# Optimization experiments

Measured on AMD Instinct MI355X. Metric: run time of the kernel, lower is better.

## Reference

```python
import jax, jax.numpy as jnp
import numpy as np
import math

TAU = 1.0  # init kwarg tau


def setup_inputs() -> dict:
    key = jax.random.key(0)
    n, m = 1024, 8192
    V = jax.random.normal(key, (n, m), dtype=jnp.float32)
    return {"V": V}


def reference(V) -> jnp.ndarray:
    n, m = V.shape
    num_rounds = math.ceil(m / n)
    # Repeat V row-blocks num_rounds times: M has shape [num_rounds*n, m]
    M = jnp.tile(V, (num_rounds, 1))

    def step(c, row):
        # Soft round-robin pick (training branch of SoftRR.__one_round)
        y = jax.nn.softmax((row - jnp.min(row) + 1.0) * c / TAU)
        c = (1.0 - y) * c
        return c, y

    c0 = jnp.ones((m,), dtype=V.dtype)
    _, R = jax.lax.scan(step, c0, M)  # R: [num_rounds*n, m]
    pi = R.reshape(num_rounds, n, m).sum(axis=0)  # [n, m]
    return pi
```

## Files before the change

kernel.cpp:

```cpp
#include <hip/hip_runtime.h>
#include <hip/hip_fp16.h>


#define N_ROWS 1024
#define M_COLS 8192
#define STEPS  8192
#define LOG2E  1.4426950408889634f

using half8  = __attribute__((ext_vector_type(8))) _Float16;
using half2v = __attribute__((ext_vector_type(2))) _Float16;
using float8 = __attribute__((ext_vector_type(8))) float;

__device__ __forceinline__ float fast_exp2(float x) {
#if __has_builtin(__builtin_amdgcn_exp2f)
  return __builtin_amdgcn_exp2f(x);
#else
  return exp2f(x);
#endif
}
__device__ __forceinline__ float fast_rcp(float x) {
#if __has_builtin(__builtin_amdgcn_rcpf)
  return __builtin_amdgcn_rcpf(x);
#else
  return 1.0f / x;
#endif
}
__device__ __forceinline__ half2v pack_f16(float y0, float y1) {
  return __builtin_bit_cast(half2v, __builtin_amdgcn_cvt_pkrtz(y0, y1));
}

template <int CTRL>
__device__ __forceinline__ float dpp_add(float x) {
  int yi = __builtin_amdgcn_update_dpp(0, __builtin_bit_cast(int, x),
                                       CTRL, 0xf, 0xf, true);
  return x + __builtin_bit_cast(float, yi);
}

__device__ __forceinline__ float wave_sum_to_lane63(float x) {
  x = dpp_add<0x111>(x);
  x = dpp_add<0x112>(x);
  x = dpp_add<0x114>(x);
  x = dpp_add<0x118>(x);
  x = dpp_add<0x142>(x);
  x = dpp_add<0x143>(x);
  return x;
}

#define BAR_LDS_ONLY() asm volatile("s_waitcnt lgkmcnt(0)\n\ts_barrier" ::: "memory")

__global__ void softrr_rowmin(const float* __restrict__ V, float* __restrict__ rmin) {
  const int row = blockIdx.x;
  const float* p = V + (size_t)row * M_COLS;
  float m = 1e30f;
  for (int j = threadIdx.x; j < M_COLS; j += 256) m = fminf(m, p[j]);
#pragma unroll
  for (int off = 32; off; off >>= 1) m = fminf(m, __shfl_xor(m, off, 64));
  __shared__ float sm[4];
  if ((threadIdx.x & 63) == 0) sm[threadIdx.x >> 6] = m;
  __syncthreads();
  if (threadIdx.x == 0) {
    rmin[row] = fminf(fminf(sm[0], sm[1]), fminf(sm[2], sm[3]));
  }
}

__global__ void softrr_prep_f32(const float* __restrict__ V, const float* __restrict__ rmin,
                                float* __restrict__ A) {
  const int idx8 = blockIdx.x * 256 + threadIdx.x;
  const int row = idx8 >> 10;
  const float mn = rmin[row];
  const float4* v4 = (const float4*)V;
  float4 va = v4[2 * idx8];
  float4 vb = v4[2 * idx8 + 1];
  float8 o;
  o[0] = (va.x - mn + 1.0f) * LOG2E;
  o[1] = (va.y - mn + 1.0f) * LOG2E;
  o[2] = (va.z - mn + 1.0f) * LOG2E;
  o[3] = (va.w - mn + 1.0f) * LOG2E;
  o[4] = (vb.x - mn + 1.0f) * LOG2E;
  o[5] = (vb.y - mn + 1.0f) * LOG2E;
  o[6] = (vb.z - mn + 1.0f) * LOG2E;
  o[7] = (vb.w - mn + 1.0f) * LOG2E;
  ((float8*)A)[idx8] = o;
}

__global__ void softrr_prep16(const float* __restrict__ V, const float* __restrict__ rmin,
                              __half* __restrict__ A) {
  const int idx8 = blockIdx.x * 256 + threadIdx.x;
  const int row = idx8 >> 10;
  const float mn = rmin[row];
  const float4* v4 = (const float4*)V;
  float4 va = v4[2 * idx8];
  float4 vb = v4[2 * idx8 + 1];
  half8 o;
  o[0] = (_Float16)((va.x - mn + 1.0f) * LOG2E);
  o[1] = (_Float16)((va.y - mn + 1.0f) * LOG2E);
  o[2] = (_Float16)((va.z - mn + 1.0f) * LOG2E);
  o[3] = (_Float16)((va.w - mn + 1.0f) * LOG2E);
  o[4] = (_Float16)((vb.x - mn + 1.0f) * LOG2E);
  o[5] = (_Float16)((vb.y - mn + 1.0f) * LOG2E);
  o[6] = (_Float16)((vb.z - mn + 1.0f) * LOG2E);
  o[7] = (_Float16)((vb.w - mn + 1.0f) * LOG2E);
  ((half8*)A)[idx8] = o;
}

template <int POS>
__device__ __forceinline__ void rr_step(
    int s,
    const float8& acur, float8& adst,
    float (&e)[8], float (&c)[8], half8& o,
    const float8* __restrict__ A8, half8* __restrict__ R8,
    float* sS, int t, int lane, int wave)
{
  if (wave == 0) sS[(POS + 2) & 3] = 0.0f;
  const float S = sS[(POS + 3) & 3];

  R8[(size_t)((s - 1) & (STEPS - 1)) * 1024 + t] = o;
  adst = A8[((s + 3) & (N_ROWS - 1)) * 1024 + t];

  const float Sinv = fast_rcp(S);

  float y[8];
#pragma unroll
  for (int k = 0; k < 8; ++k) {
    y[k] = e[k] * Sinv;
    c[k] = __builtin_fmaf(-y[k], c[k], c[k]);
    e[k] = fast_exp2(acur[k] * c[k]);
  }
  float l = ((e[0] + e[1]) + (e[2] + e[3])) + ((e[4] + e[5]) + (e[6] + e[7]));
  l = wave_sum_to_lane63(l);
  if (lane == 63) atomicAdd(&sS[POS & 3], l);

  {
    half2v h0 = pack_f16(y[0], y[1]);
    half2v h1 = pack_f16(y[2], y[3]);
    half2v h2 = pack_f16(y[4], y[5]);
    half2v h3 = pack_f16(y[6], y[7]);
    o[0] = h0[0]; o[1] = h0[1]; o[2] = h1[0]; o[3] = h1[1];
    o[4] = h2[0]; o[5] = h2[1]; o[6] = h3[0]; o[7] = h3[1];
  }
  BAR_LDS_ONLY();
}

__global__ void __launch_bounds__(1024) softrr_scan_f32(const float* __restrict__ Af,
                                                        __half* __restrict__ Rh) {
  const int t = threadIdx.x;
  const int wave = t >> 6;
  const int lane = t & 63;
  __shared__ float sS[4];

  const float8* __restrict__ A8 = (const float8*)Af;
  half8* __restrict__ R8 = (half8*)Rh;

  float c[8], e[8];
#pragma unroll
  for (int k = 0; k < 8; ++k) c[k] = 1.0f;

  if (t < 4) sS[t] = 0.0f;
  __syncthreads();

  float8 r0 = A8[t];
  float8 pA = A8[1024 + t];
  float8 pB = A8[2048 + t];
  float8 pC, pD;

#pragma unroll
  for (int k = 0; k < 8; ++k) e[k] = fast_exp2(r0[k]);
  {
    float l = ((e[0] + e[1]) + (e[2] + e[3])) + ((e[4] + e[5]) + (e[6] + e[7]));
    l = wave_sum_to_lane63(l);
    if (lane == 63) atomicAdd(&sS[3], l);
  }
  half8 o;
  {
    half2v z = pack_f16(0.0f, 0.0f);
    o[0]=z[0]; o[1]=z[1]; o[2]=z[0]; o[3]=z[1];
    o[4]=z[0]; o[5]=z[1]; o[6]=z[0]; o[7]=z[1];
  }
  BAR_LDS_ONLY();

  for (int s = 0; s < STEPS; s += 4) {
    rr_step<0>(s + 0, pA, pC, e, c, o, A8, R8, sS, t, lane, wave);
    rr_step<1>(s + 1, pB, pD, e, c, o, A8, R8, sS, t, lane, wave);
    rr_step<2>(s + 2, pC, pA, e, c, o, A8, R8, sS, t, lane, wave);
    rr_step<3>(s + 3, pD, pB, e, c, o, A8, R8, sS, t, lane, wave);
  }

  R8[(size_t)(STEPS - 1) * 1024 + t] = o;
}

__device__ __forceinline__ void rr_step16(
    int s,
    const half8& acur, half8& adst,
    float (&e)[8], float (&c)[8], half8& o,
    const half8* __restrict__ A8, half8* __restrict__ R8,
    float (*sP)[16], int t, int lane, int wave)
{
  const int par = s & 1;
  float x = (lane < 16) ? sP[par][lane] : 0.0f;
  R8[(size_t)((s - 1) & (STEPS - 1)) * 1024 + t] = o;
  adst = A8[((s + 3) & (N_ROWS - 1)) * 1024 + t];
  x = dpp_add<0x111>(x);
  x = dpp_add<0x112>(x);
  x = dpp_add<0x114>(x);
  x = dpp_add<0x118>(x);
  const float S = __builtin_bit_cast(
      float, __builtin_amdgcn_readlane(__builtin_bit_cast(int, x), 15));
  const float Sinv = fast_rcp(S);
  float y[8];
#pragma unroll
  for (int k = 0; k < 8; ++k) {
    y[k] = e[k] * Sinv;
    c[k] = __builtin_fmaf(-y[k], c[k], c[k]);
    e[k] = fast_exp2(__builtin_fmaf((float)acur[k], c[k], 0.0f));
  }
  float l = ((e[0] + e[1]) + (e[2] + e[3])) + ((e[4] + e[5]) + (e[6] + e[7]));
  l = wave_sum_to_lane63(l);
  if (lane == 63) sP[par ^ 1][wave] = l;
  {
    half2v h0 = pack_f16(y[0], y[1]);
    half2v h1 = pack_f16(y[2], y[3]);
    half2v h2 = pack_f16(y[4], y[5]);
    half2v h3 = pack_f16(y[6], y[7]);
    o[0] = h0[0]; o[1] = h0[1]; o[2] = h1[0]; o[3] = h1[1];
    o[4] = h2[0]; o[5] = h2[1]; o[6] = h3[0]; o[7] = h3[1];
  }
  BAR_LDS_ONLY();
}

__global__ void __launch_bounds__(1024) softrr_scan_nor(const __half* __restrict__ Ah,
                                                        __half* __restrict__ Rh) {
  const int t = threadIdx.x;
  const int wave = t >> 6;
  const int lane = t & 63;
  __shared__ float sP[2][16];
  const half8* __restrict__ A8 = (const half8*)Ah;
  half8* __restrict__ R8 = (half8*)Rh;
  float c[8], e[8];
#pragma unroll
  for (int k = 0; k < 8; ++k) c[k] = 1.0f;
  half8 r0 = A8[t];
  half8 pA = A8[1024 + t];
  half8 pB = A8[2048 + t];
  half8 pC, pD;
#pragma unroll
  for (int k = 0; k < 8; ++k) e[k] = fast_exp2((float)r0[k]);
  {
    float l = ((e[0] + e[1]) + (e[2] + e[3])) + ((e[4] + e[5]) + (e[6] + e[7]));
    l = wave_sum_to_lane63(l);
    if (lane == 63) sP[0][wave] = l;
  }
  half8 o;
  {
    half2v z = pack_f16(0.0f, 0.0f);
    o[0]=z[0]; o[1]=z[1]; o[2]=z[0]; o[3]=z[1];
    o[4]=z[0]; o[5]=z[1]; o[6]=z[0]; o[7]=z[1];
  }
  BAR_LDS_ONLY();
  for (int s = 0; s < STEPS; s += 4) {
    rr_step16(s + 0, pA, pC, e, c, o, A8, R8, sP, t, lane, wave);
    rr_step16(s + 1, pB, pD, e, c, o, A8, R8, sP, t, lane, wave);
    rr_step16(s + 2, pC, pA, e, c, o, A8, R8, sP, t, lane, wave);
    rr_step16(s + 3, pD, pB, e, c, o, A8, R8, sP, t, lane, wave);
  }
  R8[(size_t)(STEPS - 1) * 1024 + t] = o;
}

__global__ void softrr_sum8(const __half* __restrict__ Rh, float* __restrict__ out) {
  const int idx8 = blockIdx.x * 256 + threadIdx.x;
  const half8* R8 = (const half8*)Rh;
  float acc[8];
  {
    half8 v = R8[idx8];
#pragma unroll
    for (int k = 0; k < 8; ++k) acc[k] = (float)v[k];
  }
#pragma unroll
  for (int r = 1; r < 8; ++r) {
    half8 v = R8[(size_t)r * 1024 * 1024 + idx8];
#pragma unroll
    for (int k = 0; k < 8; ++k) acc[k] += (float)v[k];
  }
  ((float4*)out)[2 * idx8]     = make_float4(acc[0], acc[1], acc[2], acc[3]);
  ((float4*)out)[2 * idx8 + 1] = make_float4(acc[4], acc[5], acc[6], acc[7]);
}

__global__ void __launch_bounds__(1024) softrr_scan_b(const float* __restrict__ V,
                                                      const float* __restrict__ rmin,
                                                      float* __restrict__ out) {
  const int t = threadIdx.x;
  const int wave = t >> 6;
  const int lane = t & 63;
  __shared__ float partials[2][16];
  __shared__ float smin[N_ROWS];
  smin[t] = rmin[t];
  __syncthreads();
  const float4* __restrict__ V4 = (const float4*)V;
  float4* O4 = (float4*)out;
  float c[8];
#pragma unroll
  for (int k = 0; k < 8; ++k) c[k] = 1.0f;
  float4 va = V4[2 * t], vb = V4[2 * t + 1];
  float4 pa, pb;
  for (int s = 0; s < STEPS; ++s) {
    const int i = s & (N_ROWS - 1);
    const int r = s >> 10;
    const int in_ = (s + 1) & (N_ROWS - 1);
    float4 van = V4[in_ * 2048 + 2 * t];
    float4 vbn = V4[in_ * 2048 + 2 * t + 1];
    const float mn = smin[i];
    const float base = (1.0f - mn) * LOG2E;
    float vv[8] = {va.x, va.y, va.z, va.w, vb.x, vb.y, vb.z, vb.w};
    float e[8];
    float l = 0.0f;
#pragma unroll
    for (int k = 0; k < 8; ++k) {
      float zb = __builtin_fmaf(vv[k], LOG2E, base);
      e[k] = fast_exp2(zb * c[k]);
      l += e[k];
    }
#pragma unroll
    for (int off = 32; off; off >>= 1) l += __shfl_xor(l, off, 64);
    if (lane == 0) partials[s & 1][wave] = l;
    __syncthreads();
    float S = 0.0f;
#pragma unroll
    for (int w = 0; w < 16; ++w) S += partials[s & 1][w];
    const float Sinv = fast_rcp(S);
    float po[8] = {pa.x, pa.y, pa.z, pa.w, pb.x, pb.y, pb.z, pb.w};
    float o[8];
#pragma unroll
    for (int k = 0; k < 8; ++k) {
      float y = e[k] * Sinv;
      c[k] = __builtin_fmaf(-y, c[k], c[k]);
      o[k] = (r > 0) ? (po[k] + y) : y;
    }
    O4[i * 2048 + 2 * t]     = make_float4(o[0], o[1], o[2], o[3]);
    O4[i * 2048 + 2 * t + 1] = make_float4(o[4], o[5], o[6], o[7]);
    va = van; vb = vbn;
    pa = O4[in_ * 2048 + 2 * t];
    pb = O4[in_ * 2048 + 2 * t + 1];
  }
}

extern "C" void kernel_launch(void* const* d_in, const int* in_sizes, int n_in,
                              void* d_out, int out_size, void* d_ws, size_t ws_size,
                              hipStream_t stream) {
  const float* V = (const float*)d_in[0];
  float* out = (float*)d_out;
  float* rmin = (float*)d_ws;

  const size_t A16_BYTES = (size_t)N_ROWS * M_COLS * 2;
  const size_t A32_BYTES = (size_t)N_ROWS * M_COLS * 4;
  const size_t R_BYTES   = (size_t)STEPS * M_COLS * 2;
  const size_t need_f32  = 4096 + A32_BYTES + R_BYTES;
  const size_t need_nor  = 4096 + A16_BYTES + R_BYTES;

  if (ws_size >= need_f32) {
    float*  A = (float*)((char*)d_ws + 4096);
    __half* R = (__half*)((char*)d_ws + 4096 + A32_BYTES);
    softrr_rowmin<<<N_ROWS, 256, 0, stream>>>(V, rmin);
    softrr_prep_f32<<<4096, 256, 0, stream>>>(V, rmin, A);
    softrr_scan_f32<<<1, 1024, 0, stream>>>(A, R);
    softrr_sum8<<<4096, 256, 0, stream>>>(R, out);
  } else if (ws_size >= need_nor) {
    __half* A = (__half*)((char*)d_ws + 4096);
    __half* R = (__half*)((char*)d_ws + 4096 + A16_BYTES);
    softrr_rowmin<<<N_ROWS, 256, 0, stream>>>(V, rmin);
    softrr_prep16<<<4096, 256, 0, stream>>>(V, rmin, A);
    softrr_scan_nor<<<1, 1024, 0, stream>>>(A, R);
    softrr_sum8<<<4096, 256, 0, stream>>>(R, out);
  } else {
    softrr_rowmin<<<N_ROWS, 256, 0, stream>>>(V, rmin);
    softrr_scan_b<<<1, 1024, 0, stream>>>(V, rmin, out);
  }
}
```

Measured before the change: 4.865 ms.

## Replace LDS atomics with per-wave partial slots and use packed fp32 math

The single-block scan kernel now has each wave's lane 63 write its partial softmax denominator into a double-buffered per-wave LDS slot. Previously all waves did an atomicAdd into one of four rotating scalars that wave 0 had to zero each step. Every lane then reads the 16 partials and reduces them with DPP and readlane, which removes LDS atomic contention and the zeroing store. The elementwise update is also written on 2-wide float vectors so the compiler can emit packed fp32 multiply and FMA instructions. The costs are a few extra DPP operations on the serial critical path and a dependence on the compiler actually generating packed ops.

```diff
diff --git a/kernel.cpp b/kernel.cpp
--- a/kernel.cpp
+++ b/kernel.cpp
@@ -10,6 +10,7 @@
 using half8  = __attribute__((ext_vector_type(8))) _Float16;
 using half2v = __attribute__((ext_vector_type(2))) _Float16;
 using float8 = __attribute__((ext_vector_type(8))) float;
+using f32x2  = __attribute__((ext_vector_type(2))) float;
 
 __device__ __forceinline__ float fast_exp2(float x) {
 #if __has_builtin(__builtin_amdgcn_exp2f)
@@ -25,8 +26,18 @@
   return 1.0f / x;
 #endif
 }
-__device__ __forceinline__ half2v pack_f16(float y0, float y1) {
-  return __builtin_bit_cast(half2v, __builtin_amdgcn_cvt_pkrtz(y0, y1));
+__device__ __forceinline__ unsigned pack_f16_u32(float y0, float y1) {
+  return __builtin_bit_cast(unsigned, __builtin_amdgcn_cvt_pkrtz(y0, y1));
+}
+__device__ __forceinline__ f32x2 fma2(f32x2 a, f32x2 b, f32x2 c) {
+#if __has_builtin(__builtin_elementwise_fma)
+  return __builtin_elementwise_fma(a, b, c);
+#else
+  f32x2 r;
+  r[0] = __builtin_fmaf(a[0], b[0], c[0]);
+  r[1] = __builtin_fmaf(a[1], b[1], c[1]);
+  return r;
+#endif
 }
 
 template <int CTRL>
@@ -103,60 +114,68 @@
   ((half8*)A)[idx8] = o;
 }
 
-template <int POS>
-__device__ __forceinline__ void rr_step(
+__device__ __forceinline__ void rr_step_pk(
     int s,
     const float8& acur, float8& adst,
-    float (&e)[8], float (&c)[8], half8& o,
-    const float8* __restrict__ A8, half8* __restrict__ R8,
-    float* sS, int t, int lane, int wave)
+    f32x2 (&e)[4], f32x2 (&c)[4], uint4& o,
+    const float8* __restrict__ A8, uint4* __restrict__ R4,
+    float (*sP)[64], int t, int lane, int wave)
 {
-  if (wave == 0) sS[(POS + 2) & 3] = 0.0f;
-  const float S = sS[(POS + 3) & 3];
-
-  R8[(size_t)((s - 1) & (STEPS - 1)) * 1024 + t] = o;
+  const int par = s & 1;
+  float x = sP[par][lane];
+
+  R4[(size_t)((s - 1) & (STEPS - 1)) * 1024 + t] = o;
   adst = A8[((s + 3) & (N_ROWS - 1)) * 1024 + t];
 
+  x = dpp_add<0x111>(x);
+  x = dpp_add<0x112>(x);
+  x = dpp_add<0x114>(x);
+  x = dpp_add<0x118>(x);
+  const float S = __builtin_bit_cast(
+      float, __builtin_amdgcn_readlane(__builtin_bit_cast(int, x), 15));
   const float Sinv = fast_rcp(S);
-
-  float y[8];
-#pragma unroll
-  for (int k = 0; k < 8; ++k) {
-    y[k] = e[k] * Sinv;
-    c[k] = __builtin_fmaf(-y[k], c[k], c[k]);
-    e[k] = fast_exp2(acur[k] * c[k]);
-  }
-  float l = ((e[0] + e[1]) + (e[2] + e[3])) + ((e[4] + e[5]) + (e[6] + e[7]));
+  const f32x2 Sv = {Sinv, Sinv};
+
+  f32x2 y[4];
+#pragma unroll
+  for (int k = 0; k < 4; ++k) {
+    y[k] = e[k] * Sv;
+    c[k] = fma2(-y[k], c[k], c[k]);
+    f32x2 a2 = {acur[2 * k], acur[2 * k + 1]};
+    f32x2 tk = a2 * c[k];
+    e[k][0] = fast_exp2(tk[0]);
+    e[k][1] = fast_exp2(tk[1]);
+  }
+  f32x2 s01 = e[0] + e[1];
+  f32x2 s23 = e[2] + e[3];
+  f32x2 s2  = s01 + s23;
+  float l = s2[0] + s2[1];
   l = wave_sum_to_lane63(l);
-  if (lane == 63) atomicAdd(&sS[POS & 3], l);
-
-  {
-    half2v h0 = pack_f16(y[0], y[1]);
-    half2v h1 = pack_f16(y[2], y[3]);
-    half2v h2 = pack_f16(y[4], y[5]);
-    half2v h3 = pack_f16(y[6], y[7]);
-    o[0] = h0[0]; o[1] = h0[1]; o[2] = h1[0]; o[3] = h1[1];
-    o[4] = h2[0]; o[5] = h2[1]; o[6] = h3[0]; o[7] = h3[1];
-  }
+  if (lane == 63) sP[par ^ 1][wave] = l;
+
+  o.x = pack_f16_u32(y[0][0], y[0][1]);
+  o.y = pack_f16_u32(y[1][0], y[1][1]);
+  o.z = pack_f16_u32(y[2][0], y[2][1]);
+  o.w = pack_f16_u32(y[3][0], y[3][1]);
   BAR_LDS_ONLY();
 }
 
-__global__ void __launch_bounds__(1024) softrr_scan_f32(const float* __restrict__ Af,
-                                                        __half* __restrict__ Rh) {
+__global__ void __launch_bounds__(1024) softrr_scan_pk(const float* __restrict__ Af,
+                                                       __half* __restrict__ Rh) {
   const int t = threadIdx.x;
   const int wave = t >> 6;
   const int lane = t & 63;
-  __shared__ float sS[4];
+  __shared__ float sP[2][64];
 
   const float8* __restrict__ A8 = (const float8*)Af;
-  half8* __restrict__ R8 = (half8*)Rh;
-
-  float c[8], e[8];
-#pragma unroll
-  for (int k = 0; k < 8; ++k) c[k] = 1.0f;
-
-  if (t < 4) sS[t] = 0.0f;
+  uint4* __restrict__ R4 = (uint4*)Rh;
+
+  if (t < 128) ((float*)sP)[t] = 0.0f;
   __syncthreads();
+
+  f32x2 c[4], e[4];
+#pragma unroll
+  for (int k = 0; k < 4; ++k) c[k] = f32x2{1.0f, 1.0f};
 
   float8 r0 = A8[t];
   float8 pA = A8[1024 + t];
@@ -164,28 +183,33 @@
   float8 pC, pD;
 
 #pragma unroll
-  for (int k = 0; k < 8; ++k) e[k] = fast_exp2(r0[k]);
+  for (int k = 0; k < 4; ++k) {
+    e[k][0] = fast_exp2(r0[2 * k]);
+    e[k][1] = fast_exp2(r0[2 * k + 1]);
+  }
   {
-    float l = ((e[0] + e[1]) + (e[2] + e[3])) + ((e[4] + e[5]) + (e[6] + e[7]));
+    f32x2 s01 = e[0] + e[1];
+    f32x2 s23 = e[2] + e[3];
+    f32x2 s2  = s01 + s23;
+    float l = s2[0] + s2[1];
     l = wave_sum_to_lane63(l);
-    if (lane == 63) atomicAdd(&sS[3], l);
-  }
-  half8 o;
-  {
-    half2v z = pack_f16(0.0f, 0.0f);
-    o[0]=z[0]; o[1]=z[1]; o[2]=z[0]; o[3]=z[1];
-    o[4]=z[0]; o[5]=z[1]; o[6]=z[0]; o[7]=z[1];
-  }
+    if (lane == 63) sP[0][wave] = l;
+  }
+  uint4 o = make_uint4(0u, 0u, 0u, 0u);
   BAR_LDS_ONLY();
 
   for (int s = 0; s < STEPS; s += 4) {
-    rr_step<0>(s + 0, pA, pC, e, c, o, A8, R8, sS, t, lane, wave);
-    rr_step<1>(s + 1, pB, pD, e, c, o, A8, R8, sS, t, lane, wave);
-    rr_step<2>(s + 2, pC, pA, e, c, o, A8, R8, sS, t, lane, wave);
-    rr_step<3>(s + 3, pD, pB, e, c, o, A8, R8, sS, t, lane, wave);
-  }
-
-  R8[(size_t)(STEPS - 1) * 1024 + t] = o;
+    rr_step_pk(s + 0, pA, pC, e, c, o, A8, R4, sP, t, lane, wave);
+    rr_step_pk(s + 1, pB, pD, e, c, o, A8, R4, sP, t, lane, wave);
+    rr_step_pk(s + 2, pC, pA, e, c, o, A8, R4, sP, t, lane, wave);
+    rr_step_pk(s + 3, pD, pB, e, c, o, A8, R4, sP, t, lane, wave);
+  }
+
+  R4[(size_t)(STEPS - 1) * 1024 + t] = o;
+}
+
+__device__ __forceinline__ half2v pack_f16(float y0, float y1) {
+  return __builtin_bit_cast(half2v, __builtin_amdgcn_cvt_pkrtz(y0, y1));
 }
 
 __device__ __forceinline__ void rr_step16(
@@ -360,7 +384,7 @@
     __half* R = (__half*)((char*)d_ws + 4096 + A32_BYTES);
     softrr_rowmin<<<N_ROWS, 256, 0, stream>>>(V, rmin);
     softrr_prep_f32<<<4096, 256, 0, stream>>>(V, rmin, A);
-    softrr_scan_f32<<<1, 1024, 0, stream>>>(A, R);
+    softrr_scan_pk<<<1, 1024, 0, stream>>>(A, R);
     softrr_sum8<<<4096, 256, 0, stream>>>(R, out);
   } else if (ws_size >= need_nor) {
     __half* A = (__half*)((char*)d_ws + 4096);
```

After: 4.419 ms. 9.2% less time.
